# Kernel tuning notes

Measured on AMD Instinct MI355X. Metric: run time of the kernel, lower is better.

The kernel has to match this reference:

```python
import jax, jax.numpy as jnp
import numpy as np

B, VS, VO = 16, 10475, 8192
K, PS, PO = 64, 1024, 2048


def setup_inputs() -> dict:
    key = jax.random.key(0)
    k1, k2, k3, k4, k5 = jax.random.split(key, 5)
    smplx_v = jax.random.normal(k1, (B, VS, 3), dtype=jnp.float32)
    object_v = jax.random.normal(k2, (B, VO, 3), dtype=jnp.float32)
    smpl_part_idx = jax.random.randint(k3, (K, PS), 0, VS, dtype=jnp.int64) if jax.config.jax_enable_x64 else jax.random.randint(k3, (K, PS), 0, VS, dtype=jnp.int32)
    obj_part_idx = jax.random.randint(k4, (K, PO), 0, VO, dtype=jnp.int32)
    batch_idx = jax.random.randint(k5, (K,), 0, B, dtype=jnp.int32)
    return {
        'smplx_v': smplx_v,
        'object_v': object_v,
        'smpl_part_idx': smpl_part_idx,
        'obj_part_idx': obj_part_idx,
        'batch_idx': batch_idx,
    }


def reference(smplx_v, object_v, smpl_part_idx, obj_part_idx, batch_idx):
    # Batched gather of per-pair contact vertex subsets.
    sc = smplx_v[batch_idx[:, None], smpl_part_idx]   # [K, PS, 3]
    oc = object_v[batch_idx[:, None], obj_part_idx]   # [K, PO, 3]
    # Pairwise Euclidean distances [K, PS, PO] (torch.norm of differences).
    diff = sc[:, :, None, :] - oc[:, None, :, :]
    d = jnp.sqrt(jnp.sum(diff * diff, axis=-1))
    # One-directional chamfer: min over object verts, mean over smpl verts,
    # then mean over all contact pairs (torch.stack(...).mean()).
    loss = jnp.mean(jnp.mean(jnp.min(d, axis=-1), axis=-1))
    return loss
```

## Files before the change

kernel.cpp:

```cpp
#include <hip/hip_runtime.h>
#include <float.h>
#include <math.h>

constexpr int B  = 16;
constexpr int VS = 10475;
constexpr int VO = 8192;
constexpr int K  = 64;
constexpr int PS = 1024;
constexpr int PO = 2048;

constexpr int BLK  = 512;
constexpr int QPB  = 256;
constexpr int GRID = K * (PS / QPB);
constexpr int NW   = 8;
constexpr int NT   = PO / 32;

typedef float  v3f    __attribute__((ext_vector_type(3)));
typedef float  f32x16 __attribute__((ext_vector_type(16)));
typedef _Float16 half8 __attribute__((ext_vector_type(8)));
typedef unsigned int u32;
typedef u32 v4u __attribute__((ext_vector_type(4)));

__device__ __forceinline__ u32 pkh(_Float16 lo, _Float16 hi) {
    const unsigned short l = __builtin_bit_cast(unsigned short, lo);
    const unsigned short h = __builtin_bit_cast(unsigned short, hi);
    return ((u32)h << 16) | (u32)l;
}


__global__ __launch_bounds__(BLK)
void cl_onepass(const float* __restrict__ smplx_v,
                const float* __restrict__ object_v,
                const int*   __restrict__ spi,
                const int*   __restrict__ opi,
                const int*   __restrict__ bidx,
                float*       __restrict__ partial)
{
    __shared__ u32   so[(PO + 16) * 4];
    __shared__ float wsum[NW];

    const int bk   = blockIdx.x;
    const int tid  = threadIdx.x;
    const int k    = bk >> 2;
    const int ic   = bk & 3;
    const int b    = bidx[k];
    const int wave = tid >> 6;
    const int lane = tid & 63;

    const float* __restrict__ ov = object_v + (size_t)b * VO * 3;
    #pragma unroll
    for (int r = 0; r < PO / BLK; ++r) {
        const int j  = r * BLK + tid;
        const int oj = opi[k * PO + j];
        const v3f p  = *(const v3f*)(ov + 3 * (size_t)oj);
        const _Float16 hx = (_Float16)p.x, hy = (_Float16)p.y, hz = (_Float16)p.z;
        const float fx = (float)hx, fy = (float)hy, fz = (float)hz;
        const float w2 = 0.5f * (fx * fx + fy * fy + fz * fz);
        const _Float16 w2h = (_Float16)w2;
        const _Float16 w2l = (_Float16)(w2 - (float)w2h);
        const u32 d0 = pkh(hx, hy);
        *(v4u*)&so[j * 4] = (v4u){d0, pkh(hz, w2h), d0, pkh(hz, w2l)};
    }
    if (tid < 64) so[PO * 4 + tid] = 0;

    half8 afrag = (half8)(_Float16)0;
    float s2 = 0.0f;
    if (lane < 32) {
        const int i  = ic * QPB + wave * 32 + lane;
        const int si = spi[k * PS + i];
        const v3f s  = *(const v3f*)(smplx_v + 3 * ((size_t)b * VS + si));
        s2 = s.x * s.x + s.y * s.y + s.z * s.z;
        const _Float16 shx = (_Float16)s.x, shy = (_Float16)s.y, shz = (_Float16)s.z;
        const _Float16 slx = (_Float16)(s.x - (float)shx);
        const _Float16 sly = (_Float16)(s.y - (float)shy);
        const _Float16 slz = (_Float16)(s.z - (float)shz);
        const _Float16 n1  = (_Float16)(-1.0f);
        afrag = (half8){shx, shy, shz, n1, slx, sly, slz, n1};
    }
    __syncthreads();

    const u32* bp  = (lane < 32) ? &so[(lane & 31) * 4] : &so[PO * 4];
    const int  inc = (lane < 32) ? 32 * 4 : 0;

    f32x16 mint;
    #pragma unroll
    for (int i = 0; i < 16; ++i) mint[i] = FLT_MAX;

    #pragma unroll 4
    for (int t = 0; t < NT; ++t) {
        const half8 bfrag = *(const half8*)bp;
        f32x16 zc;
        #pragma unroll
        for (int i = 0; i < 16; ++i) zc[i] = 0.0f;
        const f32x16 d = __builtin_amdgcn_mfma_f32_32x32x16_f16(
            afrag, bfrag, zc, 0, 0, 0);
        #pragma unroll
        for (int i = 0; i < 16; ++i) mint[i] = fminf(mint[i], -d[i]);
        bp += inc;
    }

    #pragma unroll
    for (int m = 1; m <= 16; m <<= 1) {
        #pragma unroll
        for (int i = 0; i < 16; ++i)
            mint[i] = fminf(mint[i], __shfl_xor(mint[i], m, 64));
    }

    const int mm  = lane & 31;
    const int reg = (mm & 3) | ((mm >> 3) << 2);
    float sel = mint[0];
    #pragma unroll
    for (int r = 1; r < 16; ++r) sel = (reg == r) ? mint[r] : sel;
    const float vA = __shfl(sel, mm, 64);
    const float vB = __shfl(sel, mm + 32, 64);
    const float d2m = ((mm >> 2) & 1) ? vB : vA;

    float d = 0.0f;
    if (lane < 32)
        d = sqrtf(fmaxf(fmaf(2.0f, d2m, s2), 0.0f));

    #pragma unroll
    for (int m = 1; m <= 16; m <<= 1)
        d += __shfl_xor(d, m, 64);
    if (lane == 0) wsum[wave] = d;
    __syncthreads();

    if (tid < 64) {
        float v = (tid < NW) ? wsum[tid] : 0.0f;
        #pragma unroll
        for (int off = 4; off > 0; off >>= 1)
            v += __shfl_down(v, off, 64);
        if (tid == 0) partial[bk] = v;
    }
}


__global__ __launch_bounds__(64)
void cl_final(const float* __restrict__ partial, float* __restrict__ out)
{
    const int t = threadIdx.x;
    const float4 a = ((const float4*)partial)[t];
    float v = (a.x + a.y) + (a.z + a.w);
    #pragma unroll
    for (int off = 32; off > 0; off >>= 1)
        v += __shfl_down(v, off, 64);
    if (t == 0) out[0] = v * (1.0f / (float)(K * PS));
}


extern "C" void kernel_launch(void* const* d_in, const int* in_sizes, int n_in,
                              void* d_out, int out_size, void* d_ws, size_t ws_size,
                              hipStream_t stream)
{
    const float* smplx_v       = (const float*)d_in[0];
    const float* object_v      = (const float*)d_in[1];
    const int*   smpl_part_idx = (const int*)d_in[2];
    const int*   obj_part_idx  = (const int*)d_in[3];
    const int*   batch_idx     = (const int*)d_in[4];
    float*       out           = (float*)d_out;

    float* partial = (float*)d_ws;

    cl_onepass<<<GRID, BLK, 0, stream>>>(
        smplx_v, object_v, smpl_part_idx, obj_part_idx, batch_idx, partial);
    cl_final<<<1, 64, 0, stream>>>(partial, out);
}
```

Before: 15.68 us.

## Overlap second-half object gather with MFMA compute on first half

```diff
diff --git a/kernel.cpp b/kernel.cpp
--- a/kernel.cpp
+++ b/kernel.cpp
@@ -13,7 +13,9 @@
 constexpr int QPB  = 256;
 constexpr int GRID = K * (PS / QPB);
 constexpr int NW   = 8;
-constexpr int NT   = PO / 32;
+constexpr int HALF = PO / 2;
+constexpr int NTH  = HALF / 32;
+constexpr int OPT  = HALF / BLK;
 
 typedef float  v3f    __attribute__((ext_vector_type(3)));
 typedef float  f32x16 __attribute__((ext_vector_type(16)));
@@ -25,6 +27,16 @@
     const unsigned short l = __builtin_bit_cast(unsigned short, lo);
     const unsigned short h = __builtin_bit_cast(unsigned short, hi);
     return ((u32)h << 16) | (u32)l;
+}
+
+__device__ __forceinline__ v4u mk_entry(const v3f p) {
+    const _Float16 hx = (_Float16)p.x, hy = (_Float16)p.y, hz = (_Float16)p.z;
+    const float fx = (float)hx, fy = (float)hy, fz = (float)hz;
+    const float w2 = 0.5f * (fx * fx + fy * fy + fz * fz);
+    const _Float16 w2h = (_Float16)w2;
+    const _Float16 w2l = (_Float16)(w2 - (float)w2h);
+    const u32 d0 = pkh(hx, hy);
+    return (v4u){d0, pkh(hz, w2h), d0, pkh(hz, w2l)};
 }
 
 
@@ -47,19 +59,15 @@
     const int wave = tid >> 6;
     const int lane = tid & 63;
 
-    const float* __restrict__ ov = object_v + (size_t)b * VO * 3;
+    const float* __restrict__ ov   = object_v + (size_t)b * VO * 3;
+    const int*   __restrict__ opik = opi + k * PO;
+
     #pragma unroll
-    for (int r = 0; r < PO / BLK; ++r) {
+    for (int r = 0; r < OPT; ++r) {
         const int j  = r * BLK + tid;
-        const int oj = opi[k * PO + j];
+        const int oj = opik[j];
         const v3f p  = *(const v3f*)(ov + 3 * (size_t)oj);
-        const _Float16 hx = (_Float16)p.x, hy = (_Float16)p.y, hz = (_Float16)p.z;
-        const float fx = (float)hx, fy = (float)hy, fz = (float)hz;
-        const float w2 = 0.5f * (fx * fx + fy * fy + fz * fz);
-        const _Float16 w2h = (_Float16)w2;
-        const _Float16 w2l = (_Float16)(w2 - (float)w2h);
-        const u32 d0 = pkh(hx, hy);
-        *(v4u*)&so[j * 4] = (v4u){d0, pkh(hz, w2h), d0, pkh(hz, w2l)};
+        *(v4u*)&so[j * 4] = mk_entry(p);
     }
     if (tid < 64) so[PO * 4 + tid] = 0;
 
@@ -77,27 +85,50 @@
         const _Float16 n1  = (_Float16)(-1.0f);
         afrag = (half8){shx, shy, shz, n1, slx, sly, slz, n1};
     }
+
+    v3f p1[OPT];
+    #pragma unroll
+    for (int r = 0; r < OPT; ++r) {
+        const int oj = opik[HALF + r * BLK + tid];
+        p1[r] = *(const v3f*)(ov + 3 * (size_t)oj);
+    }
     __syncthreads();
 
-    const u32* bp  = (lane < 32) ? &so[(lane & 31) * 4] : &so[PO * 4];
-    const int  inc = (lane < 32) ? 32 * 4 : 0;
+    const int  boff = (lane < 32) ? (lane & 31) * 4 : PO * 4;
+    const int  inc  = (lane < 32) ? 32 * 4 : 0;
 
     f32x16 mint;
     #pragma unroll
     for (int i = 0; i < 16; ++i) mint[i] = FLT_MAX;
 
-    #pragma unroll 4
-    for (int t = 0; t < NT; ++t) {
-        const half8 bfrag = *(const half8*)bp;
-        f32x16 zc;
-        #pragma unroll
-        for (int i = 0; i < 16; ++i) zc[i] = 0.0f;
-        const f32x16 d = __builtin_amdgcn_mfma_f32_32x32x16_f16(
-            afrag, bfrag, zc, 0, 0, 0);
-        #pragma unroll
-        for (int i = 0; i < 16; ++i) mint[i] = fminf(mint[i], -d[i]);
-        bp += inc;
+    #define CL_TILES(BASE)                                                    \
+    {                                                                         \
+        const u32* bp = &so[(BASE) + boff];                                   \
+        _Pragma("unroll 4")                                                   \
+        for (int t = 0; t < NTH; ++t) {                                       \
+            const half8 bfrag = *(const half8*)bp;                            \
+            f32x16 zc;                                                        \
+            _Pragma("unroll")                                                 \
+            for (int i = 0; i < 16; ++i) zc[i] = 0.0f;                        \
+            const f32x16 d = __builtin_amdgcn_mfma_f32_32x32x16_f16(          \
+                afrag, bfrag, zc, 0, 0, 0);                                   \
+            _Pragma("unroll")                                                 \
+            for (int i = 0; i < 16; ++i) mint[i] = fminf(mint[i], -d[i]);     \
+            bp += inc;                                                        \
+        }                                                                     \
     }
+
+    CL_TILES(0)
+
+    #pragma unroll
+    for (int r = 0; r < OPT; ++r) {
+        const int j = HALF + r * BLK + tid;
+        *(v4u*)&so[j * 4] = mk_entry(p1[r]);
+    }
+    __syncthreads();
+
+    CL_TILES(HALF * 4)
+    #undef CL_TILES
 
     #pragma unroll
     for (int m = 1; m <= 16; m <<= 1) {
```

Result: no change. 15.59 us (median of 2 runs) (-0.6%).
